# Kernel optimization log

Hardware: AMD Instinct MI355X
Metric: run time of the kernel (lower is better)

## Reference

```python
import jax, jax.numpy as jnp
import numpy as np
import math

B, T, D, H = 4, 2048, 1024, 16
HD = D // H  # head_dim = 64

def setup_inputs() -> dict:
    key = jax.random.key(0)
    k1, k2, k3, k4, k5 = jax.random.split(key, 5)
    s = 1.0 / math.sqrt(D)
    return {
        "x": jax.random.normal(k1, (B, T, D), dtype=jnp.float32),
        "W_qkv": jax.random.normal(k2, (D, 3 * D), dtype=jnp.float32) * s,
        "b_qkv": jax.random.normal(k3, (3 * D,), dtype=jnp.float32) * 0.01,
        "W_fc": jax.random.normal(k4, (D, D), dtype=jnp.float32) * s,
        "b_fc": jax.random.normal(k5, (D,), dtype=jnp.float32) * 0.01,
    }

def reference(x, W_qkv, b_qkv, W_fc, b_fc):
    Bx, Tx, C = x.shape
    qkv = x @ W_qkv + b_qkv                                   # [B,T,3D]
    qkv = qkv.reshape(Bx, Tx, 3, H, HD)
    q, k, v = qkv[:, :, 0], qkv[:, :, 1], qkv[:, :, 2]        # [B,T,H,hd]
    scale = 1.0 / math.sqrt(HD)
    scores = jnp.einsum('bqhd,bkhd->bhqk', q, k) * scale      # [B,H,T,T]
    causal = jnp.tril(jnp.ones((Tx, Tx), dtype=bool))
    scores = jnp.where(causal, scores, -jnp.inf)
    weights = jax.nn.softmax(scores, axis=-1)
    out = jnp.einsum('bhqk,bkhd->bqhd', weights, v).reshape(Bx, Tx, C)
    return out @ W_fc + b_fc
```

## Files before the change

kernel.cpp:

```cpp
#include <hip/hip_runtime.h>
#include <hip/hip_bf16.h>

typedef __hip_bfloat16 bf16;
typedef short bf16x8 __attribute__((ext_vector_type(8)));
typedef float f32x4 __attribute__((ext_vector_type(4)));


static __device__ __forceinline__ void glds16(const bf16* g, bf16* l) {
  __builtin_amdgcn_global_load_lds(
      (const __attribute__((address_space(1))) void*)g,
      (__attribute__((address_space(3))) void*)l, 16, 0, 0);
}

static __device__ __forceinline__ unsigned short f2b(float f) {
  return __builtin_bit_cast(unsigned short, __float2bfloat16(f));
}
static __device__ __forceinline__ float b2f(unsigned int u16bits) {
  return __builtin_bit_cast(float, u16bits << 16);
}
static __device__ __forceinline__ float ex2(float x) {
  return __builtin_amdgcn_exp2f(x);
}

__global__ void k_convert(const float* __restrict__ in, unsigned short* __restrict__ out, int n4) {
  int i = blockIdx.x * 256 + threadIdx.x;
  if (i >= n4) return;
  float4 v = reinterpret_cast<const float4*>(in)[i];
  ushort4 o;
  o.x = f2b(v.x); o.y = f2b(v.y); o.z = f2b(v.z); o.w = f2b(v.w);
  reinterpret_cast<ushort4*>(out)[i] = o;
}

__global__ void k_transpose(const float* __restrict__ in, bf16* __restrict__ out, int R, int C) {
  __shared__ float t[32][33];
  int c0 = blockIdx.x * 32, r0 = blockIdx.y * 32;
  int tx = threadIdx.x, ty = threadIdx.y;
  #pragma unroll
  for (int j = 0; j < 32; j += 8)
    t[ty + j][tx] = in[(size_t)(r0 + ty + j) * C + c0 + tx];
  __syncthreads();
  #pragma unroll
  for (int j = 0; j < 32; j += 8)
    out[(size_t)(c0 + ty + j) * R + r0 + tx] = __float2bfloat16(t[tx][ty + j]);
}

template<int EPI>
__global__ __launch_bounds__(256, 2)
void k_gemm(const bf16* __restrict__ A, const bf16* __restrict__ Bt,
            const float* __restrict__ bias,
            bf16* __restrict__ Qh, bf16* __restrict__ Kh, bf16* __restrict__ Vt,
            float* __restrict__ Out)
{
  constexpr int K = 1024;
  __shared__ bf16 sA[128 * 32];
  __shared__ bf16 sB[128 * 32];
  const int tid = threadIdx.x;
  const int wv = tid >> 6, lane = tid & 63;
  const int wr = wv >> 1, wc = wv & 1;
  const int l4 = lane >> 4, l15 = lane & 15;

  const int nbx = gridDim.x;
  const int nwg = nbx * gridDim.y;
  const int flat = blockIdx.y * nbx + blockIdx.x;
  const int cpx = nwg >> 3;
  const int swz = (flat & 7) * cpx + (flat >> 3);
  const int bx = swz % nbx;
  const int by = swz / nbx;

  const int srow = lane >> 2;
  const int scol = (lane & 3) * 8;
  const bf16* gA0 = A  + (size_t)(by * 128 + wv * 16 + srow) * K + scol;
  const bf16* gB0 = Bt + (size_t)(bx * 128 + wv * 16 + srow) * K + scol;
  bf16* lA0 = sA + wv * 16 * 32;
  bf16* lB0 = sB + wv * 16 * 32;

  f32x4 acc[4][4];
  #pragma unroll
  for (int i = 0; i < 4; ++i)
    #pragma unroll
    for (int j = 0; j < 4; ++j) acc[i][j] = f32x4{0.f, 0.f, 0.f, 0.f};

  for (int kb = 0; kb < K; kb += 32) {
    glds16(gA0 + kb,                   lA0);
    glds16(gA0 + kb + (size_t)64 * K,  lA0 + 64 * 32);
    glds16(gB0 + kb,                   lB0);
    glds16(gB0 + kb + (size_t)64 * K,  lB0 + 64 * 32);
    __syncthreads();
    bf16x8 af[4], bfr[4];
    #pragma unroll
    for (int i = 0; i < 4; ++i)
      af[i] = *reinterpret_cast<const bf16x8*>(sA + (wr * 64 + i * 16 + l15) * 32 + l4 * 8);
    #pragma unroll
    for (int j = 0; j < 4; ++j)
      bfr[j] = *reinterpret_cast<const bf16x8*>(sB + (wc * 64 + j * 16 + l15) * 32 + l4 * 8);
    #pragma unroll
    for (int i = 0; i < 4; ++i)
      #pragma unroll
      for (int j = 0; j < 4; ++j)
        acc[i][j] = __builtin_amdgcn_mfma_f32_16x16x32_bf16(af[i], bfr[j], acc[i][j], 0, 0, 0);
    __syncthreads();
  }

  if (EPI == 0) {
    #pragma unroll
    for (int j = 0; j < 4; ++j) {
      const int n = bx * 128 + wc * 64 + j * 16 + l15;
      const float bj = bias[n];
      const int s = n >> 10;
      const int hh = (n >> 6) & 15;
      const int d = n & 63;
      #pragma unroll
      for (int i = 0; i < 4; ++i) {
        #pragma unroll
        for (int r = 0; r < 4; ++r) {
          const int m = by * 128 + wr * 64 + i * 16 + l4 * 4 + r;
          const int bb = m >> 11, t = m & 2047;
          const bf16 o = __float2bfloat16(acc[i][j][r] + bj);
          if (s == 0)      Qh[((size_t)((bb * 16 + hh) * 2048 + t)) * 64 + d] = o;
          else if (s == 1) Kh[((size_t)((bb * 16 + hh) * 2048 + t)) * 64 + d] = o;
          else             Vt[((size_t)((bb * 16 + hh) * 64 + d)) * 2048 + t] = o;
        }
      }
    }
  } else {
    #pragma unroll
    for (int j = 0; j < 4; ++j) {
      const int n = bx * 128 + wc * 64 + j * 16 + l15;
      const float bj = bias[n];
      #pragma unroll
      for (int i = 0; i < 4; ++i)
        #pragma unroll
        for (int r = 0; r < 4; ++r) {
          const int m = by * 128 + wr * 64 + i * 16 + l4 * 4 + r;
          Out[(size_t)m * 1024 + n] = acc[i][j][r] + bj;
        }
    }
  }
}

__global__ __launch_bounds__(256, 3)
void k_attn(const bf16* __restrict__ Qh, const bf16* __restrict__ Kh,
            const bf16* __restrict__ Vt, bf16* __restrict__ Ao)
{
  __shared__ unsigned int smem[4608];
  const int tid = threadIdx.x;
  const int wv = tid >> 6, lane = tid & 63;
  const int l4 = lane >> 4, l15 = lane & 15;

  const int bid = blockIdx.x;
  const int xcd = bid & 7;
  const int idx = bid >> 3;
  const int g   = idx & 31;
  const int grp = idx >> 5;
  const int bh  = grp * 8 + xcd;
  const int b = bh >> 4, h = bh & 15;

  const int role = (wv + bid) & 3;
  const int qi = (role < 2) ? g : (63 - g);
  const int parity = role & 1;
  const int qbase = qi * 32;

  const bf16* Qp = Qh + (size_t)bh * 2048 * 64;
  const bf16* Kp = Kh + (size_t)bh * 2048 * 64;
  const bf16* Vp = Vt + (size_t)bh * 64 * 2048;
  bf16* Pw = (bf16*)smem + wv * (32 * 72);

  bf16x8 qa[2][2];
  #pragma unroll
  for (int i = 0; i < 2; ++i)
    #pragma unroll
    for (int kh = 0; kh < 2; ++kh)
      qa[i][kh] = *reinterpret_cast<const bf16x8*>(
          Qp + (size_t)(qbase + i * 16 + l15) * 64 + kh * 32 + l4 * 8);

  f32x4 o[2][4];
  float mr[2], lr[2];
  #pragma unroll
  for (int i = 0; i < 2; ++i) {
    #pragma unroll
    for (int jd = 0; jd < 4; ++jd) o[i][jd] = f32x4{0.f, 0.f, 0.f, 0.f};
    mr[i] = -1e30f; lr[i] = 0.f;
  }

  const int ktmax = (qbase + 31) >> 6;

  const int kt0 = (parity <= ktmax) ? parity : ktmax;
  bf16x8 kbf[4][2];
  #pragma unroll
  for (int j = 0; j < 4; ++j)
    #pragma unroll
    for (int kh = 0; kh < 2; ++kh)
      kbf[j][kh] = *reinterpret_cast<const bf16x8*>(
          Kp + (size_t)(kt0 * 64 + j * 16 + l15) * 64 + kh * 32 + l4 * 8);

  for (int kt = parity; kt <= ktmax; kt += 2) {
    const bool full = (kt * 64 + 63) <= qbase;

    f32x4 s[2][4];
    #pragma unroll
    for (int i = 0; i < 2; ++i)
      #pragma unroll
      for (int j = 0; j < 4; ++j) s[i][j] = f32x4{0.f, 0.f, 0.f, 0.f};
    #pragma unroll
    for (int j = 0; j < 4; ++j)
      #pragma unroll
      for (int i = 0; i < 2; ++i) {
        s[i][j] = __builtin_amdgcn_mfma_f32_16x16x32_bf16(kbf[j][0], qa[i][0], s[i][j], 0, 0, 0);
        s[i][j] = __builtin_amdgcn_mfma_f32_16x16x32_bf16(kbf[j][1], qa[i][1], s[i][j], 0, 0, 0);
      }

    bf16x8 vbf[4][2];
    #pragma unroll
    for (int jd = 0; jd < 4; ++jd)
      #pragma unroll
      for (int kh = 0; kh < 2; ++kh)
        vbf[jd][kh] = *reinterpret_cast<const bf16x8*>(
            Vp + (size_t)(jd * 16 + l15) * 2048 + kt * 64 + kh * 32 + l4 * 8);

    #pragma unroll
    for (int i = 0; i < 2; ++i) {
      const int q = qbase + i * 16 + l15;
      #pragma unroll
      for (int j = 0; j < 4; ++j)
        #pragma unroll
        for (int r = 0; r < 4; ++r) {
          float v = s[i][j][r] * 0.18033688f;
          if (!full) {
            const int kk = kt * 64 + j * 16 + l4 * 4 + r;
            if (kk > q) v = -1e30f;
          }
          s[i][j][r] = v;
        }
    }

    float albc[2][4];
    #pragma unroll
    for (int i = 0; i < 2; ++i) {
      float mx = s[i][0][0];
      #pragma unroll
      for (int j = 0; j < 4; ++j)
        #pragma unroll
        for (int r = 0; r < 4; ++r)
          if (j + r > 0) mx = fmaxf(mx, s[i][j][r]);
      mx = fmaxf(mx, __shfl_xor(mx, 16));
      mx = fmaxf(mx, __shfl_xor(mx, 32));
      const float mn = fmaxf(mr[i], mx);
      const float al = ex2(mr[i] - mn);
      mr[i] = mn;
      float ps = 0.f;
      #pragma unroll
      for (int j = 0; j < 4; ++j) {
        const float p0 = ex2(s[i][j][0] - mn);
        const float p1 = ex2(s[i][j][1] - mn);
        const float p2 = ex2(s[i][j][2] - mn);
        const float p3 = ex2(s[i][j][3] - mn);
        ps += (p0 + p1) + (p2 + p3);
        const unsigned int u0 = (unsigned int)f2b(p0) | ((unsigned int)f2b(p1) << 16);
        const unsigned int u1 = (unsigned int)f2b(p2) | ((unsigned int)f2b(p3) << 16);
        *reinterpret_cast<uint2*>(Pw + (i * 16 + l15) * 72 + j * 16 + l4 * 4) =
            make_uint2(u0, u1);
      }
      ps += __shfl_xor(ps, 16);
      ps += __shfl_xor(ps, 32);
      lr[i] = lr[i] * al + ps;
      #pragma unroll
      for (int r = 0; r < 4; ++r) albc[i][r] = __shfl(al, l4 * 4 + r);
    }
    #pragma unroll
    for (int i = 0; i < 2; ++i)
      #pragma unroll
      for (int jd = 0; jd < 4; ++jd)
        #pragma unroll
        for (int r = 0; r < 4; ++r) o[i][jd][r] *= albc[i][r];

    const int ktn = (kt + 2 <= ktmax) ? (kt + 2) : ktmax;
    #pragma unroll
    for (int j = 0; j < 4; ++j)
      #pragma unroll
      for (int kh = 0; kh < 2; ++kh)
        kbf[j][kh] = *reinterpret_cast<const bf16x8*>(
            Kp + (size_t)(ktn * 64 + j * 16 + l15) * 64 + kh * 32 + l4 * 8);

    bf16x8 pa[2][2];
    #pragma unroll
    for (int i = 0; i < 2; ++i)
      #pragma unroll
      for (int kh = 0; kh < 2; ++kh)
        pa[i][kh] = *reinterpret_cast<const bf16x8*>(Pw + (i * 16 + l15) * 72 + kh * 32 + l4 * 8);
    #pragma unroll
    for (int jd = 0; jd < 4; ++jd)
      #pragma unroll
      for (int i = 0; i < 2; ++i) {
        o[i][jd] = __builtin_amdgcn_mfma_f32_16x16x32_bf16(pa[i][0], vbf[jd][0], o[i][jd], 0, 0, 0);
        o[i][jd] = __builtin_amdgcn_mfma_f32_16x16x32_bf16(pa[i][1], vbf[jd][1], o[i][jd], 0, 0, 0);
      }
  }

  float mrv[2][4], lrv[2][4];
  #pragma unroll
  for (int i = 0; i < 2; ++i)
    #pragma unroll
    for (int r = 0; r < 4; ++r) {
      mrv[i][r] = __shfl(mr[i], l4 * 4 + r);
      lrv[i][r] = __shfl(lr[i], l4 * 4 + r);
    }

  __syncthreads();
  unsigned int* reg0 = smem;
  unsigned int* reg1 = smem + 64 * 33;
  if (parity == 1) {
    unsigned int* p = ((role == 1) ? reg0 : reg1) + lane * 33;
    #pragma unroll
    for (int i = 0; i < 2; ++i)
      #pragma unroll
      for (int r = 0; r < 4; ++r) {
        p[i * 4 + r]     = __builtin_bit_cast(unsigned int, mrv[i][r]);
        p[8 + i * 4 + r] = __builtin_bit_cast(unsigned int, lrv[i][r]);
      }
    #pragma unroll
    for (int i = 0; i < 2; ++i)
      #pragma unroll
      for (int jd = 0; jd < 4; ++jd)
        #pragma unroll
        for (int rp = 0; rp < 2; ++rp) {
          unsigned int lo = f2b(o[i][jd][2 * rp]);
          unsigned int hi = f2b(o[i][jd][2 * rp + 1]);
          p[16 + (i * 4 + jd) * 2 + rp] = lo | (hi << 16);
        }
  }
  __syncthreads();
  if (parity == 0) {
    const unsigned int* p = ((role == 0) ? reg0 : reg1) + lane * 33;
    #pragma unroll
    for (int i = 0; i < 2; ++i)
      #pragma unroll
      for (int r = 0; r < 4; ++r) {
        const float m1 = __builtin_bit_cast(float, p[i * 4 + r]);
        const float l1 = __builtin_bit_cast(float, p[8 + i * 4 + r]);
        const float mm = fmaxf(mrv[i][r], m1);
        const float a0 = ex2(mrv[i][r] - mm);
        const float a1 = ex2(m1 - mm);
        const float inv = 1.f / (lrv[i][r] * a0 + l1 * a1);
        const int q = qbase + i * 16 + l4 * 4 + r;
        #pragma unroll
        for (int jd = 0; jd < 4; ++jd) {
          const unsigned int u = p[16 + (i * 4 + jd) * 2 + (r >> 1)];
          const float o1 = b2f((r & 1) ? (u >> 16) : (u & 0xffffu));
          const float val = (o[i][jd][r] * a0 + o1 * a1) * inv;
          Ao[(size_t)(b * 2048 + q) * 1024 + h * 64 + jd * 16 + l15] = __float2bfloat16(val);
        }
      }
  }
}

extern "C" void kernel_launch(void* const* d_in, const int* in_sizes, int n_in,
                              void* d_out, int out_size, void* d_ws, size_t ws_size,
                              hipStream_t stream)
{
  const float* x     = (const float*)d_in[0];
  const float* W_qkv = (const float*)d_in[1];
  const float* b_qkv = (const float*)d_in[2];
  const float* W_fc  = (const float*)d_in[3];
  const float* b_fc  = (const float*)d_in[4];
  float* out = (float*)d_out;

  char* ws = (char*)d_ws;
  bf16* x_bf = (bf16*)ws;  ws += (size_t)8192 * 1024 * 2;
  bf16* Wqt  = (bf16*)ws;  ws += (size_t)3072 * 1024 * 2;
  bf16* Wft  = (bf16*)ws;  ws += (size_t)1024 * 1024 * 2;
  bf16* Qh   = (bf16*)ws;  ws += (size_t)4 * 16 * 2048 * 64 * 2;
  bf16* Kh   = (bf16*)ws;  ws += (size_t)4 * 16 * 2048 * 64 * 2;
  bf16* Vt   = (bf16*)ws;  ws += (size_t)4 * 16 * 64 * 2048 * 2;
  bf16* Ao   = (bf16*)ws;  ws += (size_t)8192 * 1024 * 2;

  k_convert<<<8192, 256, 0, stream>>>(x, (unsigned short*)x_bf, 8192 * 1024 / 4);
  k_transpose<<<dim3(3072 / 32, 1024 / 32), dim3(32, 8), 0, stream>>>(W_qkv, Wqt, 1024, 3072);
  k_transpose<<<dim3(1024 / 32, 1024 / 32), dim3(32, 8), 0, stream>>>(W_fc, Wft, 1024, 1024);
  k_gemm<0><<<dim3(24, 64), 256, 0, stream>>>(x_bf, Wqt, b_qkv, Qh, Kh, Vt, nullptr);
  k_attn<<<2048, 256, 0, stream>>>(Qh, Kh, Vt, Ao);
  k_gemm<1><<<dim3(8, 64), 256, 0, stream>>>(Ao, Wft, b_fc, nullptr, nullptr, nullptr, out);
}
```

Before: 285.0 us.

## Halve attention key tile to 32 and skip rescale unless max grows by threshold

The flash-attention inner loop now processes 32 keys per step instead of 64, shrinking the score, V and P register/LDS footprint and reducing wasted work on the causal diagonal. It also adds a lazy online-softmax rescale: the running max and output accumulator are only updated when any lane's new max exceeds the old one by more than 8 (in log2 units). This removes most exponentials and accumulator multiplies, at the cost of more loop iterations and wider dynamic range in the unnormalized probabilities before bf16 conversion.

```diff
diff --git a/kernel.cpp b/kernel.cpp
--- a/kernel.cpp
+++ b/kernel.cpp
@@ -163,7 +163,7 @@
   const bf16* Qp = Qh + (size_t)bh * 2048 * 64;
   const bf16* Kp = Kh + (size_t)bh * 2048 * 64;
   const bf16* Vp = Vt + (size_t)bh * 64 * 2048;
-  bf16* Pw = (bf16*)smem + wv * (32 * 72);
+  bf16* Pw = (bf16*)smem + wv * (32 * 40);
 
   bf16x8 qa[2][2];
   #pragma unroll
@@ -182,118 +182,113 @@
     mr[i] = -1e30f; lr[i] = 0.f;
   }
 
-  const int ktmax = (qbase + 31) >> 6;
+  const int ktmax = (qbase + 31) >> 5;
 
   const int kt0 = (parity <= ktmax) ? parity : ktmax;
-  bf16x8 kbf[4][2];
-  #pragma unroll
-  for (int j = 0; j < 4; ++j)
+  bf16x8 kbf[2][2];
+  #pragma unroll
+  for (int j = 0; j < 2; ++j)
     #pragma unroll
     for (int kh = 0; kh < 2; ++kh)
       kbf[j][kh] = *reinterpret_cast<const bf16x8*>(
-          Kp + (size_t)(kt0 * 64 + j * 16 + l15) * 64 + kh * 32 + l4 * 8);
+          Kp + (size_t)(kt0 * 32 + j * 16 + l15) * 64 + kh * 32 + l4 * 8);
 
   for (int kt = parity; kt <= ktmax; kt += 2) {
-    const bool full = (kt * 64 + 63) <= qbase;
-
-    f32x4 s[2][4];
-    #pragma unroll
-    for (int i = 0; i < 2; ++i)
-      #pragma unroll
-      for (int j = 0; j < 4; ++j) s[i][j] = f32x4{0.f, 0.f, 0.f, 0.f};
-    #pragma unroll
-    for (int j = 0; j < 4; ++j)
+    const bool full = (kt * 32 + 31) <= qbase;
+
+    f32x4 s[2][2];
+    #pragma unroll
+    for (int i = 0; i < 2; ++i)
+      #pragma unroll
+      for (int j = 0; j < 2; ++j) s[i][j] = f32x4{0.f, 0.f, 0.f, 0.f};
+    #pragma unroll
+    for (int j = 0; j < 2; ++j)
       #pragma unroll
       for (int i = 0; i < 2; ++i) {
         s[i][j] = __builtin_amdgcn_mfma_f32_16x16x32_bf16(kbf[j][0], qa[i][0], s[i][j], 0, 0, 0);
         s[i][j] = __builtin_amdgcn_mfma_f32_16x16x32_bf16(kbf[j][1], qa[i][1], s[i][j], 0, 0, 0);
       }
 
-    bf16x8 vbf[4][2];
+    bf16x8 vbf[4];
     #pragma unroll
     for (int jd = 0; jd < 4; ++jd)
-      #pragma unroll
-      for (int kh = 0; kh < 2; ++kh)
-        vbf[jd][kh] = *reinterpret_cast<const bf16x8*>(
-            Vp + (size_t)(jd * 16 + l15) * 2048 + kt * 64 + kh * 32 + l4 * 8);
+      vbf[jd] = *reinterpret_cast<const bf16x8*>(
+          Vp + (size_t)(jd * 16 + l15) * 2048 + kt * 32 + l4 * 8);
 
     #pragma unroll
     for (int i = 0; i < 2; ++i) {
       const int q = qbase + i * 16 + l15;
       #pragma unroll
-      for (int j = 0; j < 4; ++j)
+      for (int j = 0; j < 2; ++j)
         #pragma unroll
         for (int r = 0; r < 4; ++r) {
           float v = s[i][j][r] * 0.18033688f;
           if (!full) {
-            const int kk = kt * 64 + j * 16 + l4 * 4 + r;
+            const int kk = kt * 32 + j * 16 + l4 * 4 + r;
             if (kk > q) v = -1e30f;
           }
           s[i][j][r] = v;
         }
     }
 
-    float albc[2][4];
     #pragma unroll
     for (int i = 0; i < 2; ++i) {
       float mx = s[i][0][0];
       #pragma unroll
-      for (int j = 0; j < 4; ++j)
+      for (int j = 0; j < 2; ++j)
         #pragma unroll
         for (int r = 0; r < 4; ++r)
           if (j + r > 0) mx = fmaxf(mx, s[i][j][r]);
       mx = fmaxf(mx, __shfl_xor(mx, 16));
       mx = fmaxf(mx, __shfl_xor(mx, 32));
-      const float mn = fmaxf(mr[i], mx);
-      const float al = ex2(mr[i] - mn);
-      mr[i] = mn;
+      if (__any(mx > mr[i] + 8.f)) {
+        const float mn = fmaxf(mr[i], mx);
+        const float al = ex2(mr[i] - mn);
+        mr[i] = mn;
+        lr[i] *= al;
+        float albc[4];
+        #pragma unroll
+        for (int r = 0; r < 4; ++r) albc[r] = __shfl(al, l4 * 4 + r);
+        #pragma unroll
+        for (int jd = 0; jd < 4; ++jd)
+          #pragma unroll
+          for (int r = 0; r < 4; ++r) o[i][jd][r] *= albc[r];
+      }
       float ps = 0.f;
       #pragma unroll
-      for (int j = 0; j < 4; ++j) {
-        const float p0 = ex2(s[i][j][0] - mn);
-        const float p1 = ex2(s[i][j][1] - mn);
-        const float p2 = ex2(s[i][j][2] - mn);
-        const float p3 = ex2(s[i][j][3] - mn);
+      for (int j = 0; j < 2; ++j) {
+        const float p0 = ex2(s[i][j][0] - mr[i]);
+        const float p1 = ex2(s[i][j][1] - mr[i]);
+        const float p2 = ex2(s[i][j][2] - mr[i]);
+        const float p3 = ex2(s[i][j][3] - mr[i]);
         ps += (p0 + p1) + (p2 + p3);
         const unsigned int u0 = (unsigned int)f2b(p0) | ((unsigned int)f2b(p1) << 16);
         const unsigned int u1 = (unsigned int)f2b(p2) | ((unsigned int)f2b(p3) << 16);
-        *reinterpret_cast<uint2*>(Pw + (i * 16 + l15) * 72 + j * 16 + l4 * 4) =
+        *reinterpret_cast<uint2*>(Pw + (i * 16 + l15) * 40 + j * 16 + l4 * 4) =
             make_uint2(u0, u1);
       }
       ps += __shfl_xor(ps, 16);
       ps += __shfl_xor(ps, 32);
-      lr[i] = lr[i] * al + ps;
-      #pragma unroll
-      for (int r = 0; r < 4; ++r) albc[i][r] = __shfl(al, l4 * 4 + r);
-    }
-    #pragma unroll
-    for (int i = 0; i < 2; ++i)
-      #pragma unroll
-      for (int jd = 0; jd < 4; ++jd)
-        #pragma unroll
-        for (int r = 0; r < 4; ++r) o[i][jd][r] *= albc[i][r];
+      lr[i] += ps;
+    }
 
     const int ktn = (kt + 2 <= ktmax) ? (kt + 2) : ktmax;
     #pragma unroll
-    for (int j = 0; j < 4; ++j)
+    for (int j = 0; j < 2; ++j)
       #pragma unroll
       for (int kh = 0; kh < 2; ++kh)
         kbf[j][kh] = *reinterpret_cast<const bf16x8*>(
-            Kp + (size_t)(ktn * 64 + j * 16 + l15) * 64 + kh * 32 + l4 * 8);
-
-    bf16x8 pa[2][2];
-    #pragma unroll
-    for (int i = 0; i < 2; ++i)
-      #pragma unroll
-      for (int kh = 0; kh < 2; ++kh)
-        pa[i][kh] = *reinterpret_cast<const bf16x8*>(Pw + (i * 16 + l15) * 72 + kh * 32 + l4 * 8);
+            Kp + (size_t)(ktn * 32 + j * 16 + l15) * 64 + kh * 32 + l4 * 8);
+
+    bf16x8 pa[2];
+    #pragma unroll
+    for (int i = 0; i < 2; ++i)
+      pa[i] = *reinterpret_cast<const bf16x8*>(Pw + (i * 16 + l15) * 40 + l4 * 8);
     #pragma unroll
     for (int jd = 0; jd < 4; ++jd)
       #pragma unroll
-      for (int i = 0; i < 2; ++i) {
-        o[i][jd] = __builtin_amdgcn_mfma_f32_16x16x32_bf16(pa[i][0], vbf[jd][0], o[i][jd], 0, 0, 0);
-        o[i][jd] = __builtin_amdgcn_mfma_f32_16x16x32_bf16(pa[i][1], vbf[jd][1], o[i][jd], 0, 0, 0);
-      }
+      for (int i = 0; i < 2; ++i)
+        o[i][jd] = __builtin_amdgcn_mfma_f32_16x16x32_bf16(pa[i], vbf[jd], o[i][jd], 0, 0, 0);
   }
 
   float mrv[2][4], lrv[2][4];
```

Result: faster. 272.9 us (-4.3%).
